# Kernel tuning notes

Measured on AMD Instinct MI355X. Metric: run time of the kernel, lower is better.

Reference implementation:

```python
import jax, jax.numpy as jnp
import numpy as np

B = 64        # batch (generation requests)
K = 3         # num_nextn_predict_layers (MTP modules == max_draft_tokens)
H = 4096      # hidden_size
V = 32000     # vocab


def _rmsnorm(x):
    return x * jax.lax.rsqrt(jnp.mean(x * x, axis=-1, keepdims=True) + 1e-6)


def setup_inputs() -> dict:
    key = jax.random.key(0)
    ks = jax.random.split(key, 8)
    logits = jax.random.normal(ks[0], (B * (K + 1), V), dtype=jnp.float32)
    hidden_states = jax.random.normal(ks[1], (B * (K + 1), H), dtype=jnp.float32)
    past_hidden_pool = jax.random.normal(ks[2], (B, K, H), dtype=jnp.float32)
    embed_tokens = jax.random.normal(ks[3], (V, H), dtype=jnp.float32) * 0.02
    lm_head = jax.random.normal(ks[4], (V, H), dtype=jnp.float32) * 0.02
    mtp_fc = jax.random.normal(ks[5], (K, 2 * H, H), dtype=jnp.float32) * 0.02
    draft_tokens = jax.random.randint(ks[6], (B, K), 0, V, dtype=jnp.int32)
    past_tokens_pool = jax.random.randint(ks[7], (B, K), 0, V, dtype=jnp.int32)
    slot_ids = jnp.arange(B, dtype=jnp.int32)
    return {
        'logits': logits, 'hidden_states': hidden_states,
        'past_hidden_pool': past_hidden_pool, 'embed_tokens': embed_tokens,
        'lm_head': lm_head, 'mtp_fc': mtp_fc, 'draft_tokens': draft_tokens,
        'past_tokens_pool': past_tokens_pool, 'slot_ids': slot_ids,
    }


def reference(logits, hidden_states, past_hidden_pool, embed_tokens, lm_head,
              mtp_fc, draft_tokens, past_tokens_pool, slot_ids):
    # ---- sample_and_accept_draft_tokens (greedy accept/reject) ----
    logits3 = logits.reshape(B, K + 1, V)
    target = jnp.argmax(logits3, axis=-1).astype(jnp.int32)          # [B, K+1]
    matches = (draft_tokens == target[:, :K]).astype(jnp.int32)      # [B, K]
    num_accepted = 1 + jnp.sum(jnp.cumprod(matches, axis=1), axis=1)  # [B]
    accepted_tokens = target                                          # [B, K+1]

    # ---- update_mtp_hidden_states: gather per-slot history, append accepted,
    #      keep last-K window ending at the golden (last accepted) token ----
    past_h = past_hidden_pool[slot_ids]                               # [B, K, H]
    past_t = past_tokens_pool[slot_ids]                               # [B, K]
    hs = hidden_states.reshape(B, K + 1, H)
    seq_h = jnp.concatenate([past_h, hs], axis=1)                     # [B, 2K+1, H]
    seq_t = jnp.concatenate([past_t, accepted_tokens], axis=1)        # [B, 2K+1]
    win = num_accepted[:, None] + jnp.arange(K, dtype=num_accepted.dtype)[None, :]
    new_past_h = jnp.take_along_axis(seq_h, win[..., None], axis=1)   # [B, K, H]
    new_past_t = jnp.take_along_axis(seq_t, win, axis=1)              # [B, K]

    # ---- MTP draft layers: fuse(norm(embed(tok)), norm(prev_hidden)) -> lm_head -> argmax ----
    golden = num_accepted - 1
    tok = jnp.take_along_axis(accepted_tokens, golden[:, None], axis=1)[:, 0]  # [B]
    h = new_past_h[:, -1]                                             # [B, H]
    drafts = []
    for j in range(K):  # fixed, small number of structurally distinct layers
        e = embed_tokens[tok]                                         # [B, H]
        x = jnp.concatenate([_rmsnorm(e), _rmsnorm(h)], axis=-1) @ mtp_fc[j]  # [B, H]
        dlog = x @ lm_head.T                                          # [B, V]
        tok = jnp.argmax(dlog, axis=-1).astype(jnp.int32)
        drafts.append(tok)
        h = x
    next_draft_tokens = jnp.stack(drafts, axis=1)                     # [B, K]
    next_new_tokens = jnp.concatenate(
        [jnp.take_along_axis(accepted_tokens, golden[:, None], axis=1),
         next_draft_tokens], axis=1)                                  # [B, K+1]
    return (accepted_tokens, num_accepted, next_draft_tokens, next_new_tokens,
            new_past_t)
```

## Files before the change

### kernel.cpp

```cpp
#include <hip/hip_runtime.h>
#include <hip/hip_bf16.h>
#include <math.h>

#define B 64
#define K 3
#define H 4096
#define V 32000
#define K1 (K + 1)

typedef short bf16x8_t __attribute__((ext_vector_type(8)));
typedef float f32x4_t __attribute__((ext_vector_type(4)));
typedef long long i64_t;

#define OFF_TARGET  0
#define OFF_TOK     1024
#define OFF_THRI    2048
#define OFF_RESK    4096
#define OFF_SCALE   8192
#define OFF_HBUF    (1u << 20)
#define OFF_XROW    (2u << 20)
#define OFF_UF      (3u << 20)
#define OFF_XF      (6u << 20)
#define OFF_DLOGA   (7u << 20)
#define OFF_PART    (16u << 20)
#define OFF_LF      (48u << 20)

#define OUT_ACC 0
#define OUT_NA  256
#define OUT_NDT 320
#define OUT_NNT 512
#define OUT_NPT 768

#define DELTA 1.5f
#define FP8SCALE 16.0f
#define INVACC (1.0f / 256.0f)

__device__ __forceinline__ unsigned short f2bf(float f) {
    unsigned int u = __float_as_uint(f);
    u += 0x7fffu + ((u >> 16) & 1u);
    return (unsigned short)(u >> 16);
}
__device__ __forceinline__ float bf2f(unsigned short h) {
    return __uint_as_float(((unsigned int)h) << 16);
}
__device__ __forceinline__ uint4 mku4(const unsigned short* p) {
    return make_uint4((unsigned)p[0] | ((unsigned)p[1] << 16),
                      (unsigned)p[2] | ((unsigned)p[3] << 16),
                      (unsigned)p[4] | ((unsigned)p[5] << 16),
                      (unsigned)p[6] | ((unsigned)p[7] << 16));
}
__device__ __forceinline__ bf16x8_t mkfrag(const unsigned short* p) {
    union { uint4 q; bf16x8_t v; } u;
    u.q = mku4(p);
    return u.v;
}
__device__ __forceinline__ unsigned fkey(float f) {
    unsigned u = __float_as_uint(f);
    return u ^ ((unsigned)((int)u >> 31) | 0x80000000u);
}
__device__ __forceinline__ float funkey(unsigned k) {
    unsigned u = (k & 0x80000000u) ? (k ^ 0x80000000u) : ~k;
    return __uint_as_float(u);
}
__device__ __forceinline__ unsigned int f2fp8(float f) {
    unsigned u = __float_as_uint(f);
    unsigned sgn = (u >> 24) & 0x80u;
    unsigned au = u & 0x7FFFFFFFu;
    if (au >= 0x43E00000u) return sgn | 0x7Eu;
    if (au < 0x3C800000u) {
        float a = __uint_as_float(au);
        int m = (int)rintf(a * 512.0f);
        return sgn | (unsigned)m;
    }
    unsigned r = au + 0x7FFFFu + ((au >> 20) & 1u);
    unsigned e = (r >> 23) - 120u;
    unsigned m = (r >> 20) & 7u;
    return sgn | (e << 3) | m;
}
__device__ __forceinline__ unsigned long long pack8fp8(const float* a) {
    unsigned lo = f2fp8(a[0]) | (f2fp8(a[1]) << 8) | (f2fp8(a[2]) << 16) | (f2fp8(a[3]) << 24);
    unsigned hi = f2fp8(a[4]) | (f2fp8(a[5]) << 8) | (f2fp8(a[6]) << 16) | (f2fp8(a[7]) << 24);
    return (unsigned long long)lo | ((unsigned long long)hi << 32);
}

__global__ void argmax_logits_kernel(const float* __restrict__ logits, int* __restrict__ target) {
    const int r = blockIdx.x;
    const float4* row = (const float4*)(logits + (size_t)r * V);
    float bv = -INFINITY;
    int bi = 0x7fffffff;
    for (int i4 = threadIdx.x; i4 < V / 4; i4 += 256) {
        float4 v = row[i4];
        int base = i4 * 4;
        if (v.x > bv) { bv = v.x; bi = base; }
        if (v.y > bv) { bv = v.y; bi = base + 1; }
        if (v.z > bv) { bv = v.z; bi = base + 2; }
        if (v.w > bv) { bv = v.w; bi = base + 3; }
    }
    __shared__ float sv[256];
    __shared__ int si[256];
    sv[threadIdx.x] = bv; si[threadIdx.x] = bi;
    __syncthreads();
    for (int s = 128; s > 0; s >>= 1) {
        if (threadIdx.x < (unsigned)s) {
            float ov = sv[threadIdx.x + s]; int oi = si[threadIdx.x + s];
            if (ov > sv[threadIdx.x] || (ov == sv[threadIdx.x] && oi < si[threadIdx.x])) {
                sv[threadIdx.x] = ov; si[threadIdx.x] = oi;
            }
        }
        __syncthreads();
    }
    if (threadIdx.x == 0) target[r] = si[0];
}

__global__ void accept_kernel(const int* __restrict__ target, const int* __restrict__ draft,
                              const int* __restrict__ past_t, const int* __restrict__ slot,
                              const float* __restrict__ hs, int* __restrict__ out,
                              int* __restrict__ tok_ws, float* __restrict__ h_buf) {
    const int b = blockIdx.x;
    __shared__ int s_na;
    if (threadIdx.x == 0) {
        const int* trow = target + b * K1;
        const int* drow = draft + b * K;
        int na = 1, prod = 1;
        for (int k = 0; k < K; ++k) { prod *= (drow[k] == trow[k]) ? 1 : 0; na += prod; }
        s_na = na;
        out[OUT_NA + b] = na;
        int srow = slot[b];
        for (int jj = 0; jj < K; ++jj) {
            int idx = na + jj;
            int v = (idx < K) ? past_t[srow * K + idx] : trow[idx - K];
            out[OUT_NPT + b * K + jj] = v;
        }
        int tok0 = trow[na - 1];
        out[OUT_NNT + b * K1 + 0] = tok0;
        tok_ws[b] = tok0;
        for (int i = 0; i < K1; ++i) out[OUT_ACC + b * K1 + i] = trow[i];
    }
    __syncthreads();
    const int na = s_na;
    const float4* src = (const float4*)(hs + ((size_t)b * K1 + (na - 1)) * H);
    float4* dst = (float4*)(h_buf + (size_t)b * H);
    for (int k = threadIdx.x; k < H / 4; k += 256) dst[k] = src[k];
}

__global__ void rms_scale_kernel(const int* __restrict__ tok_ws, const float* __restrict__ embed,
                                 const float* __restrict__ h_src, float* __restrict__ scales,
                                 unsigned int* __restrict__ thrInt, unsigned long long* __restrict__ resKey) {
    const int b = blockIdx.x, tid = threadIdx.x;
    const int tok = tok_ws[b];
    const float4* e4 = (const float4*)(embed + (size_t)tok * H);
    const float4* h4 = (const float4*)(h_src + (size_t)b * H);
    float se = 0.f, sh = 0.f;
#pragma unroll
    for (int r = 0; r < 4; ++r) {
        float4 e = e4[tid + r * 256];
        float4 h = h4[tid + r * 256];
        se += e.x * e.x + e.y * e.y + e.z * e.z + e.w * e.w;
        sh += h.x * h.x + h.y * h.y + h.z * h.z + h.w * h.w;
    }
    __shared__ float r1[256], r2[256];
    r1[tid] = se; r2[tid] = sh;
    __syncthreads();
    for (int s = 128; s > 0; s >>= 1) {
        if (tid < (unsigned)s) { r1[tid] += r1[tid + s]; r2[tid] += r2[tid + s]; }
        __syncthreads();
    }
    if (tid == 0) {
        scales[b]      = 1.0f / sqrtf(r1[0] * (1.0f / H) + 1e-6f);
        scales[64 + b] = 1.0f / sqrtf(r2[0] * (1.0f / H) + 1e-6f);
        thrInt[b] = 0u;
        resKey[b] = 0ull;
    }
}

__global__ __launch_bounds__(256) void build_uf_kernel(const int* __restrict__ tok_ws, const float* __restrict__ embed,
                                                       const float* __restrict__ h_src, const float* __restrict__ scales,
                                                       unsigned short* __restrict__ uf) {
    const int c = blockIdx.x;
    const int tid = threadIdx.x;
    const int g = tid >> 6, l = tid & 63;
    const int g4 = l >> 4, li = l & 15;
    const int b = g * 16 + li;
    unsigned short h0[8], h1[8], h2[8];
    const float* src;
    float sc;
    if (c < H / 32) { src = embed + (size_t)tok_ws[b] * H + c * 32; sc = scales[b]; }
    else            { src = h_src + (size_t)b * H + (c - H / 32) * 32; sc = scales[64 + b]; }
#pragma unroll
    for (int i = 0; i < 8; ++i) {
        const float a = src[8 * g4 + i] * sc;
        const unsigned short hh = f2bf(a);
        const float r = a - bf2f(hh);
        const unsigned short mm = f2bf(r);
        const float r2 = r - bf2f(mm);
        h0[i] = hh; h1[i] = mm; h2[i] = f2bf(r2);
    }
    unsigned short* dst = uf + (size_t)(((c * 4 + g) * 3) * 64 + l) * 8;
    *(uint4*)(dst)        = mku4(h0);
    *(uint4*)(dst + 512)  = mku4(h1);
    *(uint4*)(dst + 1024) = mku4(h2);
}

__global__ __launch_bounds__(256) void gemm1_mfma(const float* __restrict__ W,
                                                  const unsigned short* __restrict__ uf,
                                                  float* __restrict__ part) {
    const int tid = threadIdx.x, lane = tid & 63, w = tid >> 6;
    const int bx = blockIdx.x;
    const int ks = blockIdx.y;
    const int vc0 = bx * 8 + w * 2;
    const int g4 = lane >> 4, li = lane & 15;
    const int kbase = ks * 512;

    const bf16x8_t* Bu = (const bf16x8_t*)uf;
    const f32x4_t z = {0.f, 0.f, 0.f, 0.f};
    f32x4_t acc[2][4];
#pragma unroll
    for (int v2 = 0; v2 < 2; ++v2)
#pragma unroll
        for (int bc = 0; bc < 4; ++bc) acc[v2][bc] = z;

    const float* Wb = W + (size_t)(kbase + 8 * g4) * H + vc0 * 16 + li;

    float acur[2][8], anxt[2][8];
#pragma unroll
    for (int v2 = 0; v2 < 2; ++v2)
#pragma unroll
        for (int i = 0; i < 8; ++i) acur[v2][i] = Wb[(size_t)i * H + v2 * 16];

    for (int c = 0; c < 16; ++c) {
        const int cg = ks * 16 + c;
        bf16x8_t br[12];
#pragma unroll
        for (int f = 0; f < 12; ++f) br[f] = Bu[((size_t)cg * 12 + f) * 64 + lane];
        if (c + 1 < 16) {
#pragma unroll
            for (int v2 = 0; v2 < 2; ++v2)
#pragma unroll
                for (int i = 0; i < 8; ++i) anxt[v2][i] = Wb[(size_t)((c + 1) * 32 + i) * H + v2 * 16];
        }
        bf16x8_t A0[2], A1[2], A2[2];
#pragma unroll
        for (int v2 = 0; v2 < 2; ++v2) {
            unsigned short s0[8], s1[8], s2[8];
#pragma unroll
            for (int i = 0; i < 8; ++i) {
                const float a = acur[v2][i];
                const unsigned short hh = f2bf(a);
                const float r = a - bf2f(hh);
                const unsigned short mm = f2bf(r);
                const float r2 = r - bf2f(mm);
                s0[i] = hh; s1[i] = mm; s2[i] = f2bf(r2);
            }
            A0[v2] = mkfrag(s0); A1[v2] = mkfrag(s1); A2[v2] = mkfrag(s2);
        }
#pragma unroll
        for (int v2 = 0; v2 < 2; ++v2) {
#pragma unroll
            for (int bc = 0; bc < 4; ++bc) {
                f32x4_t t = acc[v2][bc];
                t = __builtin_amdgcn_mfma_f32_16x16x32_bf16(A0[v2], br[bc * 3 + 0], t, 0, 0, 0);
                t = __builtin_amdgcn_mfma_f32_16x16x32_bf16(A0[v2], br[bc * 3 + 1], t, 0, 0, 0);
                t = __builtin_amdgcn_mfma_f32_16x16x32_bf16(A1[v2], br[bc * 3 + 0], t, 0, 0, 0);
                t = __builtin_amdgcn_mfma_f32_16x16x32_bf16(A0[v2], br[bc * 3 + 2], t, 0, 0, 0);
                t = __builtin_amdgcn_mfma_f32_16x16x32_bf16(A1[v2], br[bc * 3 + 1], t, 0, 0, 0);
                t = __builtin_amdgcn_mfma_f32_16x16x32_bf16(A2[v2], br[bc * 3 + 0], t, 0, 0, 0);
                acc[v2][bc] = t;
            }
        }
#pragma unroll
        for (int v2 = 0; v2 < 2; ++v2)
#pragma unroll
            for (int i = 0; i < 8; ++i) acur[v2][i] = anxt[v2][i];
    }
#pragma unroll
    for (int v2 = 0; v2 < 2; ++v2) {
        const int obase = (vc0 + v2) * 16 + g4 * 4;
#pragma unroll
        for (int bc = 0; bc < 4; ++bc)
#pragma unroll
            for (int r = 0; r < 4; ++r)
                part[((size_t)ks * H + obase + r) * B + bc * 16 + li] = acc[v2][bc][r];
    }
}

__global__ __launch_bounds__(256) void reduce1_fused(const float* __restrict__ part, float* __restrict__ x_row,
                                                     unsigned long long* __restrict__ xf8) {
    const int kc = blockIdx.x;
    const int tid = threadIdx.x;
    const int g = tid >> 6, l = tid & 63;
    const int g4 = l >> 4, li = l & 15;
    const int b = g * 16 + li;
    __shared__ float X[32][65];
    float sv[8];
#pragma unroll
    for (int i = 0; i < 8; ++i) {
        const int o = kc * 32 + 8 * g4 + i;
        float s = 0.f;
#pragma unroll
        for (int ks = 0; ks < 16; ++ks) s += part[((size_t)ks * H + o) * B + b];
        sv[i] = s;
        X[8 * g4 + i][b] = s;
    }
    float svs[8];
#pragma unroll
    for (int i = 0; i < 8; ++i) svs[i] = sv[i] * FP8SCALE;
    xf8[(size_t)(kc * 4 + g) * 64 + l] = pack8fp8(svs);
    __syncthreads();
    const int b2 = tid >> 2, oq = tid & 3;
    float4 o0, o1;
    o0.x = X[oq * 8 + 0][b2]; o0.y = X[oq * 8 + 1][b2]; o0.z = X[oq * 8 + 2][b2]; o0.w = X[oq * 8 + 3][b2];
    o1.x = X[oq * 8 + 4][b2]; o1.y = X[oq * 8 + 5][b2]; o1.z = X[oq * 8 + 6][b2]; o1.w = X[oq * 8 + 7][b2];
    float* dst = x_row + (size_t)b2 * H + kc * 32 + oq * 8;
    *(float4*)(dst) = o0;
    *(float4*)(dst + 4) = o1;
}

__global__ __launch_bounds__(256) void gemm2_mfma_first(const float* __restrict__ L,
                                                        const unsigned long long* __restrict__ xf8,
                                                        unsigned long long* __restrict__ Lf8,
                                                        float* __restrict__ dlogA,
                                                        unsigned int* __restrict__ thrInt) {
    const int tid = threadIdx.x, lane = tid & 63, w = tid >> 6;
    const int vc = blockIdx.x * 4 + w;
    const int g4 = lane >> 4, li = lane & 15;
    const float* Lbase = L + (size_t)(vc * 16 + li) * H + 8 * g4;

    const f32x4_t z = {0.f, 0.f, 0.f, 0.f};
    f32x4_t acc[4];
#pragma unroll
    for (int g = 0; g < 4; ++g) acc[g] = z;

    float4 arf[4][2];
    unsigned long long br[4][4];
#pragma unroll
    for (int d = 0; d < 4; ++d) {
        arf[d][0] = *(const float4*)(Lbase + d * 32);
        arf[d][1] = *(const float4*)(Lbase + d * 32 + 4);
#pragma unroll
        for (int g = 0; g < 4; ++g) br[d][g] = xf8[(size_t)(d * 4 + g) * 64 + lane];
    }

    for (int kc = 0; kc < 128; kc += 4) {
#pragma unroll
        for (int d = 0; d < 4; ++d) {
            const float av[8] = {arf[d][0].x * FP8SCALE, arf[d][0].y * FP8SCALE,
                                 arf[d][0].z * FP8SCALE, arf[d][0].w * FP8SCALE,
                                 arf[d][1].x * FP8SCALE, arf[d][1].y * FP8SCALE,
                                 arf[d][1].z * FP8SCALE, arf[d][1].w * FP8SCALE};
            const unsigned long long afrag = pack8fp8(av);
            Lf8[((size_t)vc * 128 + (kc + d)) * 64 + lane] = afrag;
#pragma unroll
            for (int g = 0; g < 4; ++g)
                acc[g] = __builtin_amdgcn_mfma_f32_16x16x32_fp8_fp8((i64_t)afrag, (i64_t)br[d][g], acc[g], 0, 0, 0);
            const int nk = kc + 4 + d;
            if (nk < 128) {
                arf[d][0] = *(const float4*)(Lbase + nk * 32);
                arf[d][1] = *(const float4*)(Lbase + nk * 32 + 4);
#pragma unroll
                for (int g = 0; g < 4; ++g) br[d][g] = xf8[(size_t)(nk * 4 + g) * 64 + lane];
            }
        }
    }

    float m[4];
#pragma unroll
    for (int g = 0; g < 4; ++g) {
#pragma unroll
        for (int r = 0; r < 4; ++r) acc[g][r] *= INVACC;
        m[g] = fmaxf(fmaxf(acc[g][0], acc[g][1]), fmaxf(acc[g][2], acc[g][3]));
        m[g] = fmaxf(m[g], __shfl_xor(m[g], 16));
        m[g] = fmaxf(m[g], __shfl_xor(m[g], 32));
    }
#pragma unroll
    for (int g = 0; g < 4; ++g) {
        const int vbase = vc * 16 + g4 * 4;
#pragma unroll
        for (int r = 0; r < 4; ++r)
            dlogA[(size_t)(vbase + r) * B + g * 16 + li] = acc[g][r];
    }
    __shared__ float sm[4][4][16];
    if (lane < 16) {
#pragma unroll
        for (int g = 0; g < 4; ++g) sm[w][g][lane] = m[g];
    }
    __syncthreads();
    if (tid < 64) {
        const int gg = tid >> 4, ii = tid & 15;
        const float mm = fmaxf(fmaxf(sm[0][gg][ii], sm[1][gg][ii]), fmaxf(sm[2][gg][ii], sm[3][gg][ii]));
        atomicMax(&thrInt[tid], fkey(mm));
    }
}

__global__ __launch_bounds__(256) void gemm2_mfma(const unsigned long long* __restrict__ Lf8,
                                                  const unsigned long long* __restrict__ xf8,
                                                  float* __restrict__ dlogA,
                                                  unsigned int* __restrict__ thrInt) {
    const int tid = threadIdx.x, lane = tid & 63, w = tid >> 6;
    const int vc = blockIdx.x * 4 + w;
    const size_t aBase = (size_t)vc * 128 * 64 + lane;

    const f32x4_t z = {0.f, 0.f, 0.f, 0.f};
    f32x4_t acc[4];
#pragma unroll
    for (int g = 0; g < 4; ++g) acc[g] = z;

    unsigned long long ar[4];
    unsigned long long br[4][4];
#pragma unroll
    for (int d = 0; d < 4; ++d) {
        ar[d] = Lf8[aBase + (size_t)d * 64];
#pragma unroll
        for (int g = 0; g < 4; ++g) br[d][g] = xf8[(size_t)(d * 4 + g) * 64 + lane];
    }

    for (int kc = 0; kc < 128; kc += 4) {
#pragma unroll
        for (int d = 0; d < 4; ++d) {
#pragma unroll
            for (int g = 0; g < 4; ++g)
                acc[g] = __builtin_amdgcn_mfma_f32_16x16x32_fp8_fp8((i64_t)ar[d], (i64_t)br[d][g], acc[g], 0, 0, 0);
            const int nk = kc + 4 + d;
            if (nk < 128) {
                ar[d] = Lf8[aBase + (size_t)nk * 64];
#pragma unroll
                for (int g = 0; g < 4; ++g) br[d][g] = xf8[(size_t)(nk * 4 + g) * 64 + lane];
            }
        }
    }

    const int li = lane & 15, g4 = lane >> 4;
    float m[4];
#pragma unroll
    for (int g = 0; g < 4; ++g) {
#pragma unroll
        for (int r = 0; r < 4; ++r) acc[g][r] *= INVACC;
        m[g] = fmaxf(fmaxf(acc[g][0], acc[g][1]), fmaxf(acc[g][2], acc[g][3]));
        m[g] = fmaxf(m[g], __shfl_xor(m[g], 16));
        m[g] = fmaxf(m[g], __shfl_xor(m[g], 32));
    }
#pragma unroll
    for (int g = 0; g < 4; ++g) {
        const int vbase = vc * 16 + g4 * 4;
#pragma unroll
        for (int r = 0; r < 4; ++r)
            dlogA[(size_t)(vbase + r) * B + g * 16 + li] = acc[g][r];
    }
    __shared__ float sm[4][4][16];
    if (lane < 16) {
#pragma unroll
        for (int g = 0; g < 4; ++g) sm[w][g][lane] = m[g];
    }
    __syncthreads();
    if (tid < 64) {
        const int gg = tid >> 4, ii = tid & 15;
        const float mm = fmaxf(fmaxf(sm[0][gg][ii], sm[1][gg][ii]), fmaxf(sm[2][gg][ii], sm[3][gg][ii]));
        atomicMax(&thrInt[tid], fkey(mm));
    }
}

__global__ __launch_bounds__(256) void collect_rescore(const float* __restrict__ dlogA,
                                                       const unsigned int* __restrict__ thrInt,
                                                       const float* __restrict__ L,
                                                       const float* __restrict__ x_row,
                                                       unsigned long long* __restrict__ resKey) {
    const int v0 = blockIdx.x * 256;
    __shared__ int s_cnt;
    __shared__ int s_v[512];
    __shared__ int s_b[512];
    if (threadIdx.x == 0) s_cnt = 0;
    __syncthreads();
    for (int i = threadIdx.x; i < 256 * 64; i += 256) {
        const int vl = i >> 6, b = i & 63;
        const float val = dlogA[(size_t)(v0 + vl) * B + b];
        const float thr = funkey(thrInt[b]) - DELTA;
        if (val >= thr) {
            const int s = atomicAdd(&s_cnt, 1);
            if (s < 512) { s_v[s] = v0 + vl; s_b[s] = b; }
        }
    }
    __syncthreads();
    const int n = min(s_cnt, 512);
    const int lane = threadIdx.x & 63, w = threadIdx.x >> 6;
    for (int c = w; c < n; c += 4) {
        const int v = s_v[c], b = s_b[c];
        const float* Lr = L + (size_t)v * H;
        const float* xr = x_row + (size_t)b * H;
        float s = 0.f;
#pragma unroll 8
        for (int t = 0; t < 64; ++t) s = fmaf(Lr[lane + 64 * t], xr[lane + 64 * t], s);
#pragma unroll
        for (int off = 32; off >= 1; off >>= 1) s += __shfl_xor(s, off);
        if (lane == 0) {
            const unsigned long long key = ((unsigned long long)fkey(s) << 32) | (unsigned)(~(unsigned)v);
            atomicMax(&resKey[b], key);
        }
    }
}

__global__ void finalize_kernel(const unsigned long long* __restrict__ resKey,
                                int* __restrict__ tok_ws, int* __restrict__ out, int j) {
    const int b = threadIdx.x;
    const int v = (int)(~(unsigned)(resKey[b] & 0xFFFFFFFFull));
    tok_ws[b] = v;
    out[OUT_NDT + b * K + j] = v;
    out[OUT_NNT + b * K1 + 1 + j] = v;
}

extern "C" void kernel_launch(void* const* d_in, const int* in_sizes, int n_in,
                              void* d_out, int out_size, void* d_ws, size_t ws_size,
                              hipStream_t stream) {
    const float* logits  = (const float*)d_in[0];
    const float* hs      = (const float*)d_in[1];
    const float* embed   = (const float*)d_in[3];
    const float* lm_head = (const float*)d_in[4];
    const float* mtp_fc  = (const float*)d_in[5];
    const int* draft     = (const int*)d_in[6];
    const int* past_t    = (const int*)d_in[7];
    const int* slot      = (const int*)d_in[8];
    int* out = (int*)d_out;

    char* ws = (char*)d_ws;
    int* target          = (int*)(ws + OFF_TARGET);
    int* tok_ws          = (int*)(ws + OFF_TOK);
    unsigned int* thrInt = (unsigned int*)(ws + OFF_THRI);
    unsigned long long* resKey = (unsigned long long*)(ws + OFF_RESK);
    float* scales        = (float*)(ws + OFF_SCALE);
    float* h_buf         = (float*)(ws + OFF_HBUF);
    float* x_row         = (float*)(ws + OFF_XROW);
    unsigned short* uf   = (unsigned short*)(ws + OFF_UF);
    unsigned long long* xf8 = (unsigned long long*)(ws + OFF_XF);
    float* dlogA         = (float*)(ws + OFF_DLOGA);
    float* part          = (float*)(ws + OFF_PART);
    unsigned long long* Lf8 = (unsigned long long*)(ws + OFF_LF);

    argmax_logits_kernel<<<B * K1, 256, 0, stream>>>(logits, target);
    accept_kernel<<<B, 256, 0, stream>>>(target, draft, past_t, slot, hs, out, tok_ws, h_buf);

    for (int j = 0; j < K; ++j) {
        const float* h_src = (j == 0) ? h_buf : x_row;
        rms_scale_kernel<<<B, 256, 0, stream>>>(tok_ws, embed, h_src, scales, thrInt, resKey);
        build_uf_kernel<<<2 * H / 32, 256, 0, stream>>>(tok_ws, embed, h_src, scales, uf);
        gemm1_mfma<<<dim3(32, 16), 256, 0, stream>>>(mtp_fc + (size_t)j * 2 * H * H, uf, part);
        reduce1_fused<<<H / 32, 256, 0, stream>>>(part, x_row, xf8);
        if (j == 0)
            gemm2_mfma_first<<<V / 64, 256, 0, stream>>>(lm_head, xf8, Lf8, dlogA, thrInt);
        else
            gemm2_mfma<<<V / 64, 256, 0, stream>>>(Lf8, xf8, dlogA, thrInt);
        collect_rescore<<<V / 256, 256, 0, stream>>>(dlogA, thrInt, lm_head, x_row, resKey);
        finalize_kernel<<<1, 64, 0, stream>>>(resKey, tok_ws, out, j);
    }
}
```

Before: 606.6 us.

## Emit candidate list from gemm2 instead of full logits; halve gemm1 split-K

The gemm2 kernels no longer write the full [V,B] logit matrix. Each block now filters its own tile against its block-local max minus a margin and appends surviving (value, b, v) entries to a global candidate list through shared-memory staging. A new rescore kernel walks that compacted list, re-checks each entry against the final global threshold, and recomputes exact fp32 dot products. This removes the dense logit write and rescan, at the cost of extra atomics and a looser local threshold that may admit more candidates. Separately, gemm1's split-K factor drops from 16 to 8, so there are fewer partial sums to reduce but less parallelism.

```diff
diff --git a/kernel.cpp b/kernel.cpp
--- a/kernel.cpp
+++ b/kernel.cpp
@@ -15,13 +15,13 @@
 #define OFF_TARGET  0
 #define OFF_TOK     1024
 #define OFF_THRI    2048
+#define OFF_GCNT    3072
 #define OFF_RESK    4096
 #define OFF_SCALE   8192
 #define OFF_HBUF    (1u << 20)
 #define OFF_XROW    (2u << 20)
 #define OFF_UF      (3u << 20)
 #define OFF_XF      (6u << 20)
-#define OFF_DLOGA   (7u << 20)
 #define OFF_PART    (16u << 20)
 #define OFF_LF      (48u << 20)
 
@@ -34,6 +34,8 @@
 #define DELTA 1.5f
 #define FP8SCALE 16.0f
 #define INVACC (1.0f / 256.0f)
+#define CAPG (2000000)
+#define CAPB 2048
 
 __device__ __forceinline__ unsigned short f2bf(float f) {
     unsigned int u = __float_as_uint(f);
@@ -145,7 +147,8 @@
 
 __global__ void rms_scale_kernel(const int* __restrict__ tok_ws, const float* __restrict__ embed,
                                  const float* __restrict__ h_src, float* __restrict__ scales,
-                                 unsigned int* __restrict__ thrInt, unsigned long long* __restrict__ resKey) {
+                                 unsigned int* __restrict__ thrInt, unsigned long long* __restrict__ resKey,
+                                 int* __restrict__ gcnt) {
     const int b = blockIdx.x, tid = threadIdx.x;
     const int tok = tok_ws[b];
     const float4* e4 = (const float4*)(embed + (size_t)tok * H);
@@ -170,6 +173,7 @@
         scales[64 + b] = 1.0f / sqrtf(r2[0] * (1.0f / H) + 1e-6f);
         thrInt[b] = 0u;
         resKey[b] = 0ull;
+        if (b == 0) *gcnt = 0;
     }
 }
 
@@ -209,7 +213,7 @@
     const int ks = blockIdx.y;
     const int vc0 = bx * 8 + w * 2;
     const int g4 = lane >> 4, li = lane & 15;
-    const int kbase = ks * 512;
+    const int kbase = ks * 1024;
 
     const bf16x8_t* Bu = (const bf16x8_t*)uf;
     const f32x4_t z = {0.f, 0.f, 0.f, 0.f};
@@ -227,12 +231,12 @@
 #pragma unroll
         for (int i = 0; i < 8; ++i) acur[v2][i] = Wb[(size_t)i * H + v2 * 16];
 
-    for (int c = 0; c < 16; ++c) {
-        const int cg = ks * 16 + c;
+    for (int c = 0; c < 32; ++c) {
+        const int cg = ks * 32 + c;
         bf16x8_t br[12];
 #pragma unroll
         for (int f = 0; f < 12; ++f) br[f] = Bu[((size_t)cg * 12 + f) * 64 + lane];
-        if (c + 1 < 16) {
+        if (c + 1 < 32) {
 #pragma unroll
             for (int v2 = 0; v2 < 2; ++v2)
 #pragma unroll
@@ -297,7 +301,7 @@
         const int o = kc * 32 + 8 * g4 + i;
         float s = 0.f;
 #pragma unroll
-        for (int ks = 0; ks < 16; ++ks) s += part[((size_t)ks * H + o) * B + b];
+        for (int ks = 0; ks < 8; ++ks) s += part[((size_t)ks * H + o) * B + b];
         sv[i] = s;
         X[8 * g4 + i][b] = s;
     }
@@ -315,11 +319,13 @@
     *(float4*)(dst + 4) = o1;
 }
 
+
 __global__ __launch_bounds__(256) void gemm2_mfma_first(const float* __restrict__ L,
                                                         const unsigned long long* __restrict__ xf8,
                                                         unsigned long long* __restrict__ Lf8,
-                                                        float* __restrict__ dlogA,
-                                                        unsigned int* __restrict__ thrInt) {
+                                                        unsigned int* __restrict__ thrInt,
+                                                        int* __restrict__ gcnt,
+                                                        uint2* __restrict__ glist) {
     const int tid = threadIdx.x, lane = tid & 63, w = tid >> 6;
     const int vc = blockIdx.x * 4 + w;
     const int g4 = lane >> 4, li = lane & 15;
@@ -371,14 +377,11 @@
         m[g] = fmaxf(m[g], __shfl_xor(m[g], 16));
         m[g] = fmaxf(m[g], __shfl_xor(m[g], 32));
     }
-#pragma unroll
-    for (int g = 0; g < 4; ++g) {
-        const int vbase = vc * 16 + g4 * 4;
-#pragma unroll
-        for (int r = 0; r < 4; ++r)
-            dlogA[(size_t)(vbase + r) * B + g * 16 + li] = acc[g][r];
-    }
     __shared__ float sm[4][4][16];
+    __shared__ float bm[64];
+    __shared__ uint2 stage[CAPB];
+    __shared__ int lcnt, sbase;
+    if (tid == 0) lcnt = 0;
     if (lane < 16) {
 #pragma unroll
         for (int g = 0; g < 4; ++g) sm[w][g][lane] = m[g];
@@ -387,16 +390,42 @@
     if (tid < 64) {
         const int gg = tid >> 4, ii = tid & 15;
         const float mm = fmaxf(fmaxf(sm[0][gg][ii], sm[1][gg][ii]), fmaxf(sm[2][gg][ii], sm[3][gg][ii]));
+        bm[tid] = mm;
         atomicMax(&thrInt[tid], fkey(mm));
     }
+    __syncthreads();
+#pragma unroll
+    for (int g = 0; g < 4; ++g) {
+        const int b = g * 16 + li;
+        const float thrB = bm[b] - DELTA;
+#pragma unroll
+        for (int r = 0; r < 4; ++r) {
+            const float val = acc[g][r];
+            if (val >= thrB) {
+                const int v = vc * 16 + g4 * 4 + r;
+                const uint2 e = make_uint2(__float_as_uint(val), ((unsigned)b << 16) | (unsigned)v);
+                const int s = atomicAdd(&lcnt, 1);
+                if (s < CAPB) stage[s] = e;
+                else { const int gs = atomicAdd(gcnt, 1); if (gs < CAPG) glist[gs] = e; }
+            }
+        }
+    }
+    __syncthreads();
+    const int n = min(lcnt, CAPB);
+    if (tid == 0) sbase = atomicAdd(gcnt, n);
+    __syncthreads();
+    for (int i = tid; i < n; i += 256)
+        if (sbase + i < CAPG) glist[sbase + i] = stage[i];
 }
 
 __global__ __launch_bounds__(256) void gemm2_mfma(const unsigned long long* __restrict__ Lf8,
                                                   const unsigned long long* __restrict__ xf8,
-                                                  float* __restrict__ dlogA,
-                                                  unsigned int* __restrict__ thrInt) {
+                                                  unsigned int* __restrict__ thrInt,
+                                                  int* __restrict__ gcnt,
+                                                  uint2* __restrict__ glist) {
     const int tid = threadIdx.x, lane = tid & 63, w = tid >> 6;
     const int vc = blockIdx.x * 4 + w;
+    const int g4 = lane >> 4, li = lane & 15;
     const size_t aBase = (size_t)vc * 128 * 64 + lane;
 
     const f32x4_t z = {0.f, 0.f, 0.f, 0.f};
@@ -428,7 +457,6 @@
         }
     }
 
-    const int li = lane & 15, g4 = lane >> 4;
     float m[4];
 #pragma unroll
     for (int g = 0; g < 4; ++g) {
@@ -438,14 +466,11 @@
         m[g] = fmaxf(m[g], __shfl_xor(m[g], 16));
         m[g] = fmaxf(m[g], __shfl_xor(m[g], 32));
     }
-#pragma unroll
-    for (int g = 0; g < 4; ++g) {
-        const int vbase = vc * 16 + g4 * 4;
-#pragma unroll
-        for (int r = 0; r < 4; ++r)
-            dlogA[(size_t)(vbase + r) * B + g * 16 + li] = acc[g][r];
-    }
     __shared__ float sm[4][4][16];
+    __shared__ float bm[64];
+    __shared__ uint2 stage[CAPB];
+    __shared__ int lcnt, sbase;
+    if (tid == 0) lcnt = 0;
     if (lane < 16) {
 #pragma unroll
         for (int g = 0; g < 4; ++g) sm[w][g][lane] = m[g];
@@ -454,35 +479,47 @@
     if (tid < 64) {
         const int gg = tid >> 4, ii = tid & 15;
         const float mm = fmaxf(fmaxf(sm[0][gg][ii], sm[1][gg][ii]), fmaxf(sm[2][gg][ii], sm[3][gg][ii]));
+        bm[tid] = mm;
         atomicMax(&thrInt[tid], fkey(mm));
     }
-}
-
-__global__ __launch_bounds__(256) void collect_rescore(const float* __restrict__ dlogA,
-                                                       const unsigned int* __restrict__ thrInt,
-                                                       const float* __restrict__ L,
-                                                       const float* __restrict__ x_row,
-                                                       unsigned long long* __restrict__ resKey) {
-    const int v0 = blockIdx.x * 256;
-    __shared__ int s_cnt;
-    __shared__ int s_v[512];
-    __shared__ int s_b[512];
-    if (threadIdx.x == 0) s_cnt = 0;
-    __syncthreads();
-    for (int i = threadIdx.x; i < 256 * 64; i += 256) {
-        const int vl = i >> 6, b = i & 63;
-        const float val = dlogA[(size_t)(v0 + vl) * B + b];
-        const float thr = funkey(thrInt[b]) - DELTA;
-        if (val >= thr) {
-            const int s = atomicAdd(&s_cnt, 1);
-            if (s < 512) { s_v[s] = v0 + vl; s_b[s] = b; }
-        }
-    }
-    __syncthreads();
-    const int n = min(s_cnt, 512);
+    __syncthreads();
+#pragma unroll
+    for (int g = 0; g < 4; ++g) {
+        const int b = g * 16 + li;
+        const float thrB = bm[b] - DELTA;
+#pragma unroll
+        for (int r = 0; r < 4; ++r) {
+            const float val = acc[g][r];
+            if (val >= thrB) {
+                const int v = vc * 16 + g4 * 4 + r;
+                const uint2 e = make_uint2(__float_as_uint(val), ((unsigned)b << 16) | (unsigned)v);
+                const int s = atomicAdd(&lcnt, 1);
+                if (s < CAPB) stage[s] = e;
+                else { const int gs = atomicAdd(gcnt, 1); if (gs < CAPG) glist[gs] = e; }
+            }
+        }
+    }
+    __syncthreads();
+    const int n = min(lcnt, CAPB);
+    if (tid == 0) sbase = atomicAdd(gcnt, n);
+    __syncthreads();
+    for (int i = tid; i < n; i += 256)
+        if (sbase + i < CAPG) glist[sbase + i] = stage[i];
+}
+
+__global__ __launch_bounds__(256) void rescore_kernel(const uint2* __restrict__ glist,
+                                                      const int* __restrict__ gcnt,
+                                                      const unsigned int* __restrict__ thrInt,
+                                                      const float* __restrict__ L,
+                                                      const float* __restrict__ x_row,
+                                                      unsigned long long* __restrict__ resKey) {
+    const int total = min(*gcnt, CAPG);
     const int lane = threadIdx.x & 63, w = threadIdx.x >> 6;
-    for (int c = w; c < n; c += 4) {
-        const int v = s_v[c], b = s_b[c];
+    for (int idx = blockIdx.x * 4 + w; idx < total; idx += gridDim.x * 4) {
+        const uint2 e = glist[idx];
+        const int b = (int)(e.y >> 16), v = (int)(e.y & 0xFFFFu);
+        const float aval = __uint_as_float(e.x);
+        if (aval < funkey(thrInt[b]) - DELTA) continue;
         const float* Lr = L + (size_t)v * H;
         const float* xr = x_row + (size_t)b * H;
         float s = 0.f;
@@ -523,14 +560,15 @@
     int* target          = (int*)(ws + OFF_TARGET);
     int* tok_ws          = (int*)(ws + OFF_TOK);
     unsigned int* thrInt = (unsigned int*)(ws + OFF_THRI);
+    int* gcnt            = (int*)(ws + OFF_GCNT);
     unsigned long long* resKey = (unsigned long long*)(ws + OFF_RESK);
     float* scales        = (float*)(ws + OFF_SCALE);
     float* h_buf         = (float*)(ws + OFF_HBUF);
     float* x_row         = (float*)(ws + OFF_XROW);
     unsigned short* uf   = (unsigned short*)(ws + OFF_UF);
     unsigned long long* xf8 = (unsigned long long*)(ws + OFF_XF);
-    float* dlogA         = (float*)(ws + OFF_DLOGA);
     float* part          = (float*)(ws + OFF_PART);
+    uint2* glist         = (uint2*)(ws + OFF_PART);
     unsigned long long* Lf8 = (unsigned long long*)(ws + OFF_LF);
 
     argmax_logits_kernel<<<B * K1, 256, 0, stream>>>(logits, target);
@@ -538,15 +576,15 @@
 
     for (int j = 0; j < K; ++j) {
         const float* h_src = (j == 0) ? h_buf : x_row;
-        rms_scale_kernel<<<B, 256, 0, stream>>>(tok_ws, embed, h_src, scales, thrInt, resKey);
+        rms_scale_kernel<<<B, 256, 0, stream>>>(tok_ws, embed, h_src, scales, thrInt, resKey, gcnt);
         build_uf_kernel<<<2 * H / 32, 256, 0, stream>>>(tok_ws, embed, h_src, scales, uf);
-        gemm1_mfma<<<dim3(32, 16), 256, 0, stream>>>(mtp_fc + (size_t)j * 2 * H * H, uf, part);
+        gemm1_mfma<<<dim3(32, 8), 256, 0, stream>>>(mtp_fc + (size_t)j * 2 * H * H, uf, part);
         reduce1_fused<<<H / 32, 256, 0, stream>>>(part, x_row, xf8);
         if (j == 0)
-            gemm2_mfma_first<<<V / 64, 256, 0, stream>>>(lm_head, xf8, Lf8, dlogA, thrInt);
+            gemm2_mfma_first<<<V / 64, 256, 0, stream>>>(lm_head, xf8, Lf8, thrInt, gcnt, glist);
         else
-            gemm2_mfma<<<V / 64, 256, 0, stream>>>(Lf8, xf8, dlogA, thrInt);
-        collect_rescore<<<V / 256, 256, 0, stream>>>(dlogA, thrInt, lm_head, x_row, resKey);
+            gemm2_mfma<<<V / 64, 256, 0, stream>>>(Lf8, xf8, thrInt, gcnt, glist);
+        rescore_kernel<<<256, 256, 0, stream>>>(glist, gcnt, thrInt, lm_head, x_row, resKey);
         finalize_kernel<<<1, 64, 0, stream>>>(resKey, tok_ws, out, j);
     }
 }
```

Measured after the change: 665.4 us. 9.7% more time.
